# Kernel optimization log

Measured on AMD Instinct MI355X. Metric: run time of the kernel, lower is better.

The kernel has to match this reference:

```python
import jax, jax.numpy as jnp
import numpy as np

QMAX_ACT = 127.0  # int8 symmetric token-wise activation quant


def _dequant_weight(qweight, zeros, qstep, base_scales, step_scales):
    # qweight: [OC, IC] int in [0,16); zeros/qstep: [OC, G] int; base/step scales: [OC]
    OC, IC = qweight.shape
    G = qstep.shape[1]
    gs = IC // G
    # per (oc, g) scale reconstructed from base + quantized step decomposition
    scales = base_scales[:, None] + step_scales[:, None] * qstep.astype(jnp.float32)  # [OC, G]
    w = (qweight.reshape(OC, G, gs).astype(jnp.float32) - zeros.astype(jnp.float32)[:, :, None]) * scales[:, :, None]
    return w.reshape(OC, IC)


def _tokenwise_quant(x):
    # symmetric per-token int8 quantization
    amax = jnp.max(jnp.abs(x), axis=-1, keepdims=True)  # [B, S, 1]
    x_scales = amax / QMAX_ACT
    qx = jnp.clip(jnp.round(x / jnp.maximum(x_scales, 1e-8)), -QMAX_ACT, QMAX_ACT)
    return qx, x_scales


def setup_inputs() -> dict:
    key = jax.random.key(0)
    k1, k2, k3, k4, k5, k6 = jax.random.split(key, 6)
    B, S, IC, OC, G = 4, 2048, 4096, 4096, 32
    x = jax.random.normal(k1, (B, S, IC), dtype=jnp.float32)
    qweight = jax.random.randint(k2, (OC, IC), 0, 16, dtype=jnp.int32)
    zeros = jax.random.randint(k3, (OC, G), 0, 16, dtype=jnp.int32)
    qstep = jax.random.randint(k4, (OC, G), 0, 16, dtype=jnp.int32)
    base_scales = jax.random.uniform(k5, (OC,), dtype=jnp.float32) * 0.01 + 1e-4
    step_scales = jax.random.uniform(k6, (OC,), dtype=jnp.float32) * 0.001
    return {"x": x, "qweight": qweight, "zeros": zeros, "qstep": qstep,
            "base_scales": base_scales, "step_scales": step_scales}


def reference(x, qweight, zeros, qstep, base_scales, step_scales):
    # Faithful QuantLinear forward: token-wise int8 activation quant, then
    # GEMM against grouped int4 weight dequantized with base+step scale decomposition.
    W = _dequant_weight(qweight, zeros, qstep, base_scales, step_scales)  # [OC, IC]
    qx, x_scales = _tokenwise_quant(x)  # [B,S,IC], [B,S,1]
    out = jnp.einsum('bsi,oi->bso', qx, W) * x_scales  # fused dequant-GEMM semantics
    return out
```

## Files before the change

### kernel.cpp

```cpp
#include <hip/hip_runtime.h>
#include <hip/hip_bf16.h>

typedef int   i32x4 __attribute__((ext_vector_type(4)));
typedef float f32x4 __attribute__((ext_vector_type(4)));

constexpr int K_IC = 4096;
constexpr int N_OC = 4096;
constexpr int GROUPS = 32;

__global__ __launch_bounds__(256) void prep_kernel(const float* __restrict__ x,
                                                   const int* __restrict__ qweight,
                                                   const int* __restrict__ zeros,
                                                   const int* __restrict__ qstep,
                                                   const float* __restrict__ base_scales,
                                                   const float* __restrict__ step_scales,
                                                   char* __restrict__ qx8,
                                                   char* __restrict__ w8,
                                                   float* __restrict__ sT,
                                                   float* __restrict__ x_scales,
                                                   int M) {
    const int tid = threadIdx.x;
    if ((int)blockIdx.x < M) {
        const int m = blockIdx.x;
        const float4* xr = (const float4*)(x + (size_t)m * K_IC);
        float4 v[4];
        float amax = 0.f;
#pragma unroll
        for (int i = 0; i < 4; ++i) {
            v[i] = xr[i * 256 + tid];
            amax = fmaxf(amax, fmaxf(fmaxf(fabsf(v[i].x), fabsf(v[i].y)),
                                     fmaxf(fabsf(v[i].z), fabsf(v[i].w))));
        }
#pragma unroll
        for (int off = 32; off > 0; off >>= 1)
            amax = fmaxf(amax, __shfl_xor(amax, off, 64));
        __shared__ float wmax[4];
        if ((tid & 63) == 0) wmax[tid >> 6] = amax;
        __syncthreads();
        amax = fmaxf(fmaxf(wmax[0], wmax[1]), fmaxf(wmax[2], wmax[3]));

        const float scale = amax / 127.0f;
        if (tid == 0) x_scales[m] = scale;
        const float inv = 1.0f / fmaxf(scale, 1e-8f);

        char4* qr = (char4*)(qx8 + (size_t)m * K_IC);
#pragma unroll
        for (int i = 0; i < 4; ++i) {
            char4 o;
            o.x = (char)(int)fminf(fmaxf(rintf(v[i].x * inv), -127.f), 127.f);
            o.y = (char)(int)fminf(fmaxf(rintf(v[i].y * inv), -127.f), 127.f);
            o.z = (char)(int)fminf(fmaxf(rintf(v[i].z * inv), -127.f), 127.f);
            o.w = (char)(int)fminf(fmaxf(rintf(v[i].w * inv), -127.f), 127.f);
            qr[i * 256 + tid] = o;
        }
    } else {
        const int oc = blockIdx.x - M;
        const int4* qwr = (const int4*)(qweight + (size_t)oc * K_IC);
        char4* wr = (char4*)(w8 + (size_t)oc * K_IC);
#pragma unroll
        for (int i = 0; i < 4; ++i) {
            const int idx = i * 256 + tid;
            const int g = idx >> 5;
            const int zp = zeros[oc * GROUPS + g];
            int4 a = qwr[idx];
            char4 o;
            o.x = (char)(a.x - zp); o.y = (char)(a.y - zp);
            o.z = (char)(a.z - zp); o.w = (char)(a.w - zp);
            wr[idx] = o;
        }
        if (tid < GROUPS) {
            sT[(size_t)tid * N_OC + oc] =
                base_scales[oc] + step_scales[oc] * (float)qstep[oc * GROUPS + tid];
        }
    }
}

#define BM 256
#define BN 256
#define BK 128

__device__ inline void async16(const char* g, char* l) {
    __builtin_amdgcn_global_load_lds(
        (const __attribute__((address_space(1))) void*)g,
        (__attribute__((address_space(3))) void*)l,
        16, 0, 0);
}

__global__ __launch_bounds__(512, 2) void gemm_kernel(const char* __restrict__ A8,
                                                      const char* __restrict__ B8,
                                                      const float* __restrict__ sT,
                                                      const float* __restrict__ x_scales,
                                                      float* __restrict__ out) {
    __shared__ __attribute__((aligned(16))) char As[2][BM][BK];
    __shared__ __attribute__((aligned(16))) char Bs[2][BN][BK];

    const int tid  = threadIdx.x;
    const int lane = tid & 63;
    const int wave = tid >> 6;
    const int waveM = wave >> 2;
    const int waveN = wave & 3;

    const int GX   = N_OC / BN;
    const int flat = blockIdx.y * GX + blockIdx.x;
    const int nwg  = GX * gridDim.y;
    int swz = flat;
    if ((nwg & 7) == 0) swz = (flat & 7) * (nwg >> 3) + (flat >> 3);
    const int bn = swz & (GX - 1);
    const int bm = swz / GX;

    f32x4 accF[8][4] = {};
    const i32x4 zeroq = {0, 0, 0, 0};

    const int rowInB = tid >> 3;
    const int chunk  = tid & 7;
    const int srcOff = ((chunk ^ (rowInB & 7)) * 16);
    const char* Ap = A8 + (size_t)(bm * BM + rowInB) * K_IC + srcOff;
    const char* Bp = B8 + (size_t)(bn * BN + rowInB) * K_IC + srcOff;

    auto STAGE = [&](int b, int t) {
        const int k0 = t * BK;
#pragma unroll
        for (int i = 0; i < 4; ++i)
            async16(Ap + (size_t)(i * 64) * K_IC + k0, &As[b][rowInB + i * 64][chunk * 16]);
#pragma unroll
        for (int i = 0; i < 4; ++i)
            async16(Bp + (size_t)(i * 64) * K_IC + k0, &Bs[b][rowInB + i * 64][chunk * 16]);
    };

    const int mrow = waveM * 128 + (lane & 15);
    const int nrow = waveN * 64 + (lane & 15);
    const int q    = lane >> 4;
    const int sw   = lane & 7;
    const int colBase = bn * BN + waveN * 64 + (lane & 15);

    float scolC[4], scolN[4];
    {
        const float* sg = sT + colBase;
#pragma unroll
        for (int j = 0; j < 4; ++j) scolN[j] = sg[j * 16];
    }

    STAGE(0, 0);

    for (int t = 0; t < GROUPS; ++t) {
        const int c = t & 1;
        __syncthreads();
        if (t + 1 < GROUPS) STAGE(c ^ 1, t + 1);

#pragma unroll
        for (int j = 0; j < 4; ++j) scolC[j] = scolN[j];
        if (t + 1 < GROUPS) {
            const float* sg = sT + (size_t)(t + 1) * N_OC + colBase;
#pragma unroll
            for (int j = 0; j < 4; ++j) scolN[j] = sg[j * 16];
        }

        i32x4 bq[4][2];
#pragma unroll
        for (int j = 0; j < 4; ++j)
#pragma unroll
            for (int kk = 0; kk < 2; ++kk)
                bq[j][kk] = *(const i32x4*)&Bs[c][nrow + j * 16][((kk * 4 + q) ^ sw) * 16];

#pragma unroll
        for (int ph = 0; ph < 4; ++ph) {
            const int m0 = mrow + (2 * ph) * 16;
            const int m1 = mrow + (2 * ph + 1) * 16;
            i32x4 a0k0 = *(const i32x4*)&As[c][m0][((0 + q) ^ sw) * 16];
            i32x4 a0k1 = *(const i32x4*)&As[c][m0][((4 + q) ^ sw) * 16];
            i32x4 a1k0 = *(const i32x4*)&As[c][m1][((0 + q) ^ sw) * 16];
            i32x4 a1k1 = *(const i32x4*)&As[c][m1][((4 + q) ^ sw) * 16];

            i32x4 p[8];
            __builtin_amdgcn_s_setprio(1);
#pragma unroll
            for (int j = 0; j < 4; ++j)
                p[j] = __builtin_amdgcn_mfma_i32_16x16x64_i8(a0k0, bq[j][0], zeroq, 0, 0, 0);
#pragma unroll
            for (int j = 0; j < 4; ++j)
                p[4 + j] = __builtin_amdgcn_mfma_i32_16x16x64_i8(a1k0, bq[j][0], zeroq, 0, 0, 0);
#pragma unroll
            for (int j = 0; j < 4; ++j)
                p[j] = __builtin_amdgcn_mfma_i32_16x16x64_i8(a0k1, bq[j][1], p[j], 0, 0, 0);
#pragma unroll
            for (int j = 0; j < 4; ++j)
                p[4 + j] = __builtin_amdgcn_mfma_i32_16x16x64_i8(a1k1, bq[j][1], p[4 + j], 0, 0, 0);
            __builtin_amdgcn_s_setprio(0);

#pragma unroll
            for (int j = 0; j < 4; ++j)
#pragma unroll
                for (int r = 0; r < 4; ++r) {
                    accF[2 * ph][j][r]     += scolC[j] * (float)p[j][r];
                    accF[2 * ph + 1][j][r] += scolC[j] * (float)p[4 + j][r];
                }
        }
    }

    const int colT = lane & 15;
    const int rgrp = lane >> 4;
#pragma unroll
    for (int i = 0; i < 8; ++i) {
#pragma unroll
        for (int r = 0; r < 4; ++r) {
            const int gr = bm * BM + waveM * 128 + i * 16 + rgrp * 4 + r;
            const float sc = x_scales[gr];
#pragma unroll
            for (int j = 0; j < 4; ++j) {
                const int gc = bn * BN + waveN * 64 + j * 16 + colT;
                out[(size_t)gr * N_OC + gc] = accF[i][j][r] * sc;
            }
        }
    }
}

extern "C" void kernel_launch(void* const* d_in, const int* in_sizes, int n_in,
                              void* d_out, int out_size, void* d_ws, size_t ws_size,
                              hipStream_t stream) {
    const float* x          = (const float*)d_in[0];
    const int*   qweight    = (const int*)d_in[1];
    const int*   zeros      = (const int*)d_in[2];
    const int*   qstep      = (const int*)d_in[3];
    const float* base_scale = (const float*)d_in[4];
    const float* step_scale = (const float*)d_in[5];
    float* out = (float*)d_out;

    const int M = in_sizes[0] / K_IC;

    char* ws = (char*)d_ws;
    char*  qx8 = ws;
    char*  w8  = ws + (size_t)M * K_IC;
    float* sT  = (float*)(w8 + (size_t)N_OC * K_IC);
    float* xs  = sT + (size_t)GROUPS * N_OC;

    prep_kernel<<<M + N_OC, 256, 0, stream>>>(x, qweight, zeros, qstep,
                                              base_scale, step_scale,
                                              qx8, w8, sT, xs, M);

    dim3 grid(N_OC / BN, M / BM);
    gemm_kernel<<<grid, 512, 0, stream>>>(qx8, w8, sT, xs, out);
}
```

Measured before the change: 450.4 us.

## Interleave async tile loads across MFMA phases with explicit waitcnt pipelining

Splits the global-to-LDS staging of A and B into halves and spreads them over the four compute phases of each K step. B is now prefetched two steps ahead into the buffer just consumed, and explicit vmcnt/lgkmcnt waits plus s_barrier calls replace the single __syncthreads per step. The goal is to hide memory latency behind MFMA work and smooth out bursts of load issue. In exchange there are more barriers per iteration, and the hand-tuned waitcnt counts are fragile: correctness depends on the exact number of outstanding loads and on the buffer reuse ordering.

```diff
diff --git a/kernel.cpp b/kernel.cpp
--- a/kernel.cpp
+++ b/kernel.cpp
@@ -117,14 +117,17 @@
     const char* Ap = A8 + (size_t)(bm * BM + rowInB) * K_IC + srcOff;
     const char* Bp = B8 + (size_t)(bn * BN + rowInB) * K_IC + srcOff;
 
-    auto STAGE = [&](int b, int t) {
+    auto stageA = [&](int b, int t, int half) {
         const int k0 = t * BK;
-#pragma unroll
-        for (int i = 0; i < 4; ++i)
-            async16(Ap + (size_t)(i * 64) * K_IC + k0, &As[b][rowInB + i * 64][chunk * 16]);
-#pragma unroll
-        for (int i = 0; i < 4; ++i)
-            async16(Bp + (size_t)(i * 64) * K_IC + k0, &Bs[b][rowInB + i * 64][chunk * 16]);
+        const int i0 = 2 * half;
+        async16(Ap + (size_t)(i0 * 64) * K_IC + k0, &As[b][rowInB + i0 * 64][chunk * 16]);
+        async16(Ap + (size_t)((i0 + 1) * 64) * K_IC + k0, &As[b][rowInB + (i0 + 1) * 64][chunk * 16]);
+    };
+    auto stageB = [&](int b, int t, int half) {
+        const int k0 = t * BK;
+        const int i0 = 2 * half;
+        async16(Bp + (size_t)(i0 * 64) * K_IC + k0, &Bs[b][rowInB + i0 * 64][chunk * 16]);
+        async16(Bp + (size_t)((i0 + 1) * 64) * K_IC + k0, &Bs[b][rowInB + (i0 + 1) * 64][chunk * 16]);
     };
 
     const int mrow = waveM * 128 + (lane & 15);
@@ -134,43 +137,63 @@
     const int colBase = bn * BN + waveN * 64 + (lane & 15);
 
     float scolC[4], scolN[4];
+
+    stageA(0, 0, 0); stageA(0, 0, 1);
+    stageB(0, 0, 0); stageB(0, 0, 1);
+    stageB(1, 1, 0); stageB(1, 1, 1);
     {
         const float* sg = sT + colBase;
 #pragma unroll
-        for (int j = 0; j < 4; ++j) scolN[j] = sg[j * 16];
-    }
-
-    STAGE(0, 0);
-
+        for (int j = 0; j < 4; ++j) scolC[j] = sg[j * 16];
+    }
+    __builtin_amdgcn_sched_barrier(0);
+    asm volatile("s_waitcnt vmcnt(0)" ::: "memory");
+    __builtin_amdgcn_sched_barrier(0);
+    __builtin_amdgcn_s_barrier();
+
+#pragma unroll 1
     for (int t = 0; t < GROUPS; ++t) {
         const int c = t & 1;
-        __syncthreads();
-        if (t + 1 < GROUPS) STAGE(c ^ 1, t + 1);
-
-#pragma unroll
-        for (int j = 0; j < 4; ++j) scolC[j] = scolN[j];
-        if (t + 1 < GROUPS) {
-            const float* sg = sT + (size_t)(t + 1) * N_OC + colBase;
-#pragma unroll
-            for (int j = 0; j < 4; ++j) scolN[j] = sg[j * 16];
-        }
-
         i32x4 bq[4][2];
-#pragma unroll
-        for (int j = 0; j < 4; ++j)
-#pragma unroll
-            for (int kk = 0; kk < 2; ++kk)
-                bq[j][kk] = *(const i32x4*)&Bs[c][nrow + j * 16][((kk * 4 + q) ^ sw) * 16];
 
 #pragma unroll
         for (int ph = 0; ph < 4; ++ph) {
+            if (ph == 0) {
+#pragma unroll
+                for (int j = 0; j < 4; ++j)
+#pragma unroll
+                    for (int kk = 0; kk < 2; ++kk)
+                        bq[j][kk] = *(const i32x4*)&Bs[c][nrow + j * 16][((kk * 4 + q) ^ sw) * 16];
+            }
             const int m0 = mrow + (2 * ph) * 16;
-            const int m1 = mrow + (2 * ph + 1) * 16;
+            const int m1 = m0 + 16;
             i32x4 a0k0 = *(const i32x4*)&As[c][m0][((0 + q) ^ sw) * 16];
             i32x4 a0k1 = *(const i32x4*)&As[c][m0][((4 + q) ^ sw) * 16];
             i32x4 a1k0 = *(const i32x4*)&As[c][m1][((0 + q) ^ sw) * 16];
             i32x4 a1k1 = *(const i32x4*)&As[c][m1][((4 + q) ^ sw) * 16];
 
+            if (ph == 0 && t + 1 < GROUPS) {
+                stageA(c ^ 1, t + 1, 0);
+                const float* sg = sT + (size_t)(t + 1) * N_OC + colBase;
+#pragma unroll
+                for (int j = 0; j < 4; ++j) scolN[j] = sg[j * 16];
+            }
+            if (ph == 1 && t + 1 < GROUPS) stageA(c ^ 1, t + 1, 1);
+            if (ph == 2 && t + 2 < GROUPS) stageB(c, t + 2, 0);
+            if (ph == 3) {
+                if (t + 2 < GROUPS) {
+                    stageB(c, t + 2, 1);
+                    __builtin_amdgcn_sched_barrier(0);
+                    asm volatile("s_waitcnt vmcnt(4)" ::: "memory");
+                } else if (t + 1 < GROUPS) {
+                    asm volatile("s_waitcnt vmcnt(0)" ::: "memory");
+                }
+            }
+            __builtin_amdgcn_sched_barrier(0);
+            __builtin_amdgcn_s_barrier();
+            asm volatile("s_waitcnt lgkmcnt(0)" ::: "memory");
+            __builtin_amdgcn_sched_barrier(0);
+
             i32x4 p[8];
             __builtin_amdgcn_s_setprio(1);
 #pragma unroll
@@ -194,6 +217,12 @@
                     accF[2 * ph][j][r]     += scolC[j] * (float)p[j][r];
                     accF[2 * ph + 1][j][r] += scolC[j] * (float)p[4 + j][r];
                 }
+            __builtin_amdgcn_s_barrier();
+        }
+
+        if (t + 1 < GROUPS) {
+#pragma unroll
+            for (int j = 0; j < 4; ++j) scolC[j] = scolN[j];
         }
     }
 
```

Result: slower. 1.105 ms (+145.3%).
